# Kernel tuning notes

Hardware: AMD Instinct MI355X
Metric: run time of the kernel (lower is better)

Reference implementation:

```python
import jax, jax.numpy as jnp
import numpy as np

NUM_GROUPS = 4
DIVERSITY_STRENGTH = -0.5   # module stores -diversity_strength
DIVERSITY_DISCOUNT = 0.5
CAND_MULT = 1
N_GRAM = 2


def setup_inputs() -> dict:
    key = jax.random.key(0)
    k1, k2, k3, k5, k6 = jax.random.split(key, 5)
    bsz, beam, vocab, T = 64, 8, 50257, 128
    return {
        "lprobs": jax.random.normal(k1, (bsz, beam, vocab), jnp.float32),
        "scores": jax.random.normal(k2, (bsz, beam, T), jnp.float32),
        "group_overlap": jax.random.uniform(k3, (bsz, NUM_GROUPS, NUM_GROUPS), jnp.float32),
        "original_batch_idxs": jnp.arange(bsz, dtype=jnp.int32),
        "last_n_gram_indices": jax.random.randint(k5, (bsz, beam, N_GRAM - 1), 0, vocab, jnp.int32),
        "mask_last_n_gram_indices": jax.random.randint(k6, (bsz, beam, N_GRAM), 0, 2, jnp.int32),
        "step": 5,
    }


def reference(lprobs, scores, group_overlap, original_batch_idxs,
              last_n_gram_indices, mask_last_n_gram_indices, step):
    bsz, beam, vocab = lprobs.shape
    G = NUM_GROUPS
    mb = beam // G  # mini beam size
    k = CAND_MULT * mb
    batch_ar = jnp.arange(bsz)[:, None]

    scores_G, beams_G, idx_G = [], [], []
    for g in range(G):
        lp = lprobs[:, g::G, :]                       # [bsz, mb, vocab]
        sc = scores[:, g::G, step - 1]                # [bsz, mb]
        mk = mask_last_n_gram_indices[:, g::G, :]     # [bsz, mb, n_gram]
        if g > 0:
            # diversity penalty: scatter-add (1 + overlap) at previously picked tokens
            pen = 1.0 + group_overlap[original_batch_idxs, g, :g]          # [bsz, g]
            src = jnp.broadcast_to(pen[:, None, :], (bsz, mb, g)).reshape(bsz, -1)
            prev_idx = jnp.stack(idx_G, axis=-1).reshape(bsz, -1)          # [bsz, mb*g]
            div = jnp.zeros((bsz, vocab), lp.dtype).at[batch_ar, prev_idx].add(src)
            lp = lp + DIVERSITY_STRENGTH * div[:, None, :]
        # n-gram overlap mask: zero out beams whose mask rows are not all ones
        valid = (mk.sum(-1) == N_GRAM)                # [bsz, mb]
        lp = jnp.where(valid[:, :, None], lp, 0.0)
        # step > 0: add accumulated beam scores
        lp = lp + sc[:, :, None]
        flat = lp.reshape(bsz, -1)                    # [bsz, mb*vocab]
        top_idx = jax.lax.top_k(flat, k)[1]
        top_val = jnp.take_along_axis(flat, top_idx, axis=-1)
        beams_G.append((top_idx // vocab) * G + g)
        idx_G.append(top_idx % vocab)
        scores_G.append(top_val)

    scores_buf = jnp.stack(scores_G, axis=2).reshape(bsz, -1)   # [bsz, beam]
    indices_buf = jnp.stack(idx_G, axis=2).reshape(bsz, -1)
    beams_buf = jnp.stack(beams_G, axis=2).reshape(bsz, -1)

    # Hamming-cumulative overlap: [bsz, beam, n_gram] present n-grams, grouped
    present = jnp.concatenate(
        [last_n_gram_indices, indices_buf[:, :, None]], axis=-1
    ).reshape(bsz, mb, G, N_GRAM)
    eq = (present[:, :, None, :, :] == present[:, :, :, None, :])  # [bsz, mb, G, G, n]
    m = (mask_last_n_gram_indices != 0).reshape(bsz, mb, G, N_GRAM)
    om = m[:, :, None, :, :] & m[:, :, :, None, :]
    eq = jnp.where(om, eq, False)
    ov = (eq.sum(-1) == N_GRAM).astype(jnp.int32).sum(1)           # [bsz, G, G]

    new_group_overlap = (
        group_overlap.at[original_batch_idxs].add(ov.astype(group_overlap.dtype))
        * DIVERSITY_DISCOUNT
    )
    return scores_buf, indices_buf, beams_buf, new_group_overlap
```

## Files before the change

kernel.cpp:

```cpp
#include <hip/hip_runtime.h>
#include <math.h>

#define VOCAB 50257
#define BSZ   64
#define BEAM  8
#define NG    4
#define MB    2
#define KC    2
#define TLEN  128
#define NGRAM 2
#define SEG    64
#define SEGLEN 786
#define ROWS  (BSZ * BEAM)
#define CAP   1024

__device__ __forceinline__ bool better(float v1, int i1, float v2, int i2) {
    return (v1 > v2) || (v1 == v2 && i1 < i2);
}

struct Top2 { float v1, v2; int i1, i2; };

__device__ __forceinline__ void t2_init(Top2& t) {
    t.v1 = -INFINITY; t.v2 = -INFINITY; t.i1 = 0x7FFFFFFF; t.i2 = 0x7FFFFFFF;
}

__device__ __forceinline__ void t2_push(Top2& t, float v, int i) {
    if (better(v, i, t.v2, t.i2)) {
        if (better(v, i, t.v1, t.i1)) { t.v2 = t.v1; t.i2 = t.i1; t.v1 = v; t.i1 = i; }
        else                          { t.v2 = v;    t.i2 = i; }
    }
}

__device__ __forceinline__ void t2_merge(Top2& a, const Top2& b) {
    if (better(b.v1, b.i1, a.v1, a.i1)) {
        float nv2; int ni2;
        if (better(a.v1, a.i1, b.v2, b.i2)) { nv2 = a.v1; ni2 = a.i1; }
        else                                { nv2 = b.v2; ni2 = b.i2; }
        a.v1 = b.v1; a.i1 = b.i1; a.v2 = nv2; a.i2 = ni2;
    } else {
        if (better(b.v1, b.i1, a.v2, a.i2)) { a.v2 = b.v1; a.i2 = b.i1; }
    }
}

__device__ __forceinline__ float max4(float4 v) {
    return fmaxf(fmaxf(v.x, v.y), fmaxf(v.z, v.w));
}

__global__ __launch_bounds__(1024) void dbs_candidates(
    const float* __restrict__ lprobs,
    const int*   __restrict__ mask,
    int*   __restrict__ wscnt,
    float* __restrict__ wscv,
    int*   __restrict__ wsci)
{
    const int r    = blockIdx.x;
    const int tid  = threadIdx.x;
    const int w    = tid >> 6, lane = tid & 63;

    if (mask[r * NGRAM] + mask[r * NGRAM + 1] != NGRAM) return;

    __shared__ float s_max[SEG];
    __shared__ float s_tau;
    __shared__ int   s_cnt;
    __shared__ float s_cv[CAP];
    __shared__ int   s_ci[CAP];

    if (tid == 0) s_cnt = 0;

    const size_t rowoff = (size_t)r * VOCAB;
    const float* row = lprobs + rowoff;

    #pragma unroll
    for (int s = 0; s < 4; ++s) {
        const int seg   = w * 4 + s;
        const int start = seg * SEGLEN;
        const int end   = min(start + SEGLEN, VOCAB);
        const int mis   = (int)((rowoff + start) & 3);
        const int pre   = (4 - mis) & 3;

        float m = -INFINITY;
        if (lane < pre && start + lane < end) m = row[start + lane];
        const int vstart = start + pre;
        const int n4 = (end > vstart) ? ((end - vstart) >> 2) : 0;
        const float4* vrow = (const float4*)(row + vstart);

        float a0 = -INFINITY, a1 = -INFINITY, a2 = -INFINITY, a3 = -INFINITY;
        if (lane       < n4) a0 = max4(vrow[lane]);
        if (lane +  64 < n4) a1 = max4(vrow[lane + 64]);
        if (lane + 128 < n4) a2 = max4(vrow[lane + 128]);
        if (lane + 192 < n4) a3 = max4(vrow[lane + 192]);
        m = fmaxf(m, fmaxf(fmaxf(a0, a1), fmaxf(a2, a3)));
        const int tstart = vstart + 4 * n4;
        if (tstart + lane < end) m = fmaxf(m, row[tstart + lane]);

        #pragma unroll
        for (int off = 32; off > 0; off >>= 1) m = fmaxf(m, __shfl_xor(m, off));
        if (lane == 0) s_max[seg] = m;
    }
    __syncthreads();

    if (w == 0) {
        const float mym = s_max[lane];
        int rank = 0;
        for (int i = 0; i < SEG; ++i) {
            const float om = __shfl(mym, i);
            rank += better(om, i, mym, lane) ? 1 : 0;
        }
        if (rank == 7) s_tau = mym;
    }
    __syncthreads();
    const float tau = s_tau;

    #pragma unroll
    for (int s = 0; s < 4; ++s) {
        const int seg   = w * 4 + s;
        const int start = seg * SEGLEN;
        const int end   = min(start + SEGLEN, VOCAB);
        const int mis   = (int)((rowoff + start) & 3);
        const int pre   = (4 - mis) & 3;

        if (lane < pre && start + lane < end) {
            const float v = row[start + lane];
            if (v >= tau) {
                const int p = atomicAdd(&s_cnt, 1);
                if (p < CAP) { s_cv[p] = v; s_ci[p] = start + lane; }
            }
        }
        const int vstart = start + pre;
        const int n4 = (end > vstart) ? ((end - vstart) >> 2) : 0;
        const float4* vrow = (const float4*)(row + vstart);

        #pragma unroll
        for (int u = 0; u < 4; ++u) {
            const int jj = lane + u * 64;
            if (jj < n4) {
                const float4 v = vrow[jj];
                if (max4(v) >= tau) {
                    const int base = vstart + 4 * jj;
                    #pragma unroll
                    for (int e = 0; e < 4; ++e) {
                        const float ve = (e == 0) ? v.x : (e == 1) ? v.y
                                       : (e == 2) ? v.z : v.w;
                        if (ve >= tau) {
                            const int p = atomicAdd(&s_cnt, 1);
                            if (p < CAP) { s_cv[p] = ve; s_ci[p] = base + e; }
                        }
                    }
                }
            }
        }
        const int tstart = vstart + 4 * n4;
        if (tstart + lane < end) {
            const float v = row[tstart + lane];
            if (v >= tau) {
                const int p = atomicAdd(&s_cnt, 1);
                if (p < CAP) { s_cv[p] = v; s_ci[p] = tstart + lane; }
            }
        }
    }
    __syncthreads();

    const int cnt = min(s_cnt, CAP);
    if (tid == 0) wscnt[r] = cnt;
    for (int c = tid; c < cnt; c += 1024) {
        wscv[(size_t)r * CAP + c] = s_cv[c];
        wsci[(size_t)r * CAP + c] = s_ci[c];
    }
}

__global__ __launch_bounds__(64) void dbs_final(
    const float* __restrict__ scores,
    const float* __restrict__ overlap,
    const int*   __restrict__ obi,
    const int*   __restrict__ lastn,
    const int*   __restrict__ mask,
    const int*   __restrict__ stepp,
    const int*   __restrict__ wscnt,
    const float* __restrict__ wscv,
    const int*   __restrict__ wsci,
    float*       __restrict__ out)
{
    const int b   = blockIdx.x;
    const int tid = threadIdx.x;
    const int step = stepp[0];
    const int ob   = obi[b];

    __shared__ float s_sc[BEAM];
    __shared__ int   s_valid[BEAM];
    __shared__ float s_pen[(NG-1)*KC];
    __shared__ int   s_penidx[(NG-1)*KC];
    __shared__ float s_selv[NG][KC];
    __shared__ int   s_seli[NG][KC];
    __shared__ int   s_selm[NG][KC];

    if (tid < BEAM) {
        const int* mk = mask + ((size_t)b * BEAM + tid) * NGRAM;
        s_valid[tid] = (mk[0] + mk[1]) == NGRAM;
        s_sc[tid]    = scores[((size_t)b * BEAM + tid) * TLEN + (step - 1)];
    }
    __syncthreads();

    for (int g = 0; g < NG; ++g) {
        if (tid == 0) {
            for (int j = 0; j < g; ++j) {
                const float pen = 1.0f + overlap[((size_t)ob * NG + g) * NG + j];
                s_penidx[j*KC + 0] = s_seli[j][0]; s_pen[j*KC + 0] = pen;
                s_penidx[j*KC + 1] = s_seli[j][1]; s_pen[j*KC + 1] = pen;
            }
        }
        __syncthreads();

        const int np = KC * g;
        Top2 t; t2_init(t);
        for (int m = 0; m < MB; ++m) {
            const int beam = m * NG + g;
            if (s_valid[beam]) {
                const int r = b * BEAM + beam;
                const int n = wscnt[r];
                for (int c = tid; c < n; c += 64) {
                    const float v   = wscv[(size_t)r * CAP + c];
                    const int   idx = wsci[(size_t)r * CAP + c];
                    float dv = 0.0f;
                    #pragma unroll
                    for (int p = 0; p < (NG-1)*KC; ++p)
                        if (p < np && s_penidx[p] == idx) dv += s_pen[p];
                    t2_push(t, v - 0.5f * dv + s_sc[beam], m * VOCAB + idx);
                }
            } else if (tid < KC) {
                t2_push(t, s_sc[beam], m * VOCAB + tid);
            }
        }

        #pragma unroll
        for (int off = 32; off > 0; off >>= 1) {
            Top2 o;
            o.v1 = __shfl_down(t.v1, off); o.i1 = __shfl_down(t.i1, off);
            o.v2 = __shfl_down(t.v2, off); o.i2 = __shfl_down(t.i2, off);
            t2_merge(t, o);
        }
        if (tid == 0) {
            s_selv[g][0] = t.v1; s_seli[g][0] = t.i1 % VOCAB; s_selm[g][0] = t.i1 / VOCAB;
            s_selv[g][1] = t.v2; s_seli[g][1] = t.i2 % VOCAB; s_selm[g][1] = t.i2 / VOCAB;
        }
        __syncthreads();
    }

    if (tid < KC * NG) {
        const int i = tid;
        const int m = i / NG, g = i % NG;
        out[(size_t)b * BEAM + i]        = s_selv[g][m];
        out[512 + (size_t)b * BEAM + i]  = (float)s_seli[g][m];
        out[1024 + (size_t)b * BEAM + i] = (float)(s_selm[g][m] * NG + g);
    }
    if (tid >= 16 && tid < 16 + NG * NG) {
        const int q  = tid - 16;
        const int g1 = q / NG, g2 = q % NG;
        int ov = 0;
        for (int m = 0; m < MB; ++m) {
            const int i1 = m * NG + g1, i2 = m * NG + g2;
            const int p1a = lastn[(size_t)b * BEAM + i1];
            const int p2a = lastn[(size_t)b * BEAM + i2];
            const int p1b = s_seli[g1][m];
            const int p2b = s_seli[g2][m];
            const int* mk1 = mask + ((size_t)b * BEAM + i1) * NGRAM;
            const int* mk2 = mask + ((size_t)b * BEAM + i2) * NGRAM;
            const bool e0 = (p1a == p2a) && (mk1[0] != 0) && (mk2[0] != 0);
            const bool e1 = (p1b == p2b) && (mk1[1] != 0) && (mk2[1] != 0);
            ov += (e0 && e1) ? 1 : 0;
        }
        out[1536 + (size_t)ob * (NG * NG) + q] =
            (overlap[(size_t)ob * (NG * NG) + q] + (float)ov) * 0.5f;
    }
}

extern "C" void kernel_launch(void* const* d_in, const int* in_sizes, int n_in,
                              void* d_out, int out_size, void* d_ws, size_t ws_size,
                              hipStream_t stream) {
    const float* lprobs  = (const float*)d_in[0];
    const float* scores  = (const float*)d_in[1];
    const float* overlap = (const float*)d_in[2];
    const int*   obi     = (const int*)d_in[3];
    const int*   lastn   = (const int*)d_in[4];
    const int*   mask    = (const int*)d_in[5];
    const int*   stepp   = (const int*)d_in[6];
    float*       out     = (float*)d_out;

    int*   wscnt = (int*)d_ws;
    float* wscv  = (float*)((char*)d_ws + ROWS * 4);
    int*   wsci  = (int*)((char*)d_ws + ROWS * 4 + (size_t)ROWS * CAP * 4);

    dbs_candidates<<<ROWS, 1024, 0, stream>>>(lprobs, mask, wscnt, wscv, wsci);
    dbs_final     <<<BSZ, 64, 0, stream>>>(scores, overlap, obi, lastn, mask, stepp,
                                           wscnt, wscv, wsci, out);
}
```

Before: 27.20 us.

## Split each row's candidate filtering across four 256-thread blocks

Instead of one 1024-thread block per row computing a threshold over 64 segments, each row is now handled by four 256-thread blocks, each covering 16 segments with its own local threshold (8th-largest segment max) and its own candidate buffer. The final kernel then merges candidates from all four quarter-slots. The aim is finer-grained blocks for better CU occupancy and scheduling, and less shared memory per block. The cost is more candidates overall, since each quarter keeps at least 8 segments' worth, and a longer merge loop in the final kernel.

```diff
diff --git a/kernel.cpp b/kernel.cpp
--- a/kernel.cpp
+++ b/kernel.cpp
@@ -9,10 +9,11 @@
 #define KC    2
 #define TLEN  128
 #define NGRAM 2
-#define SEG    64
 #define SEGLEN 786
+#define QSEG  16
+#define NQ    4
 #define ROWS  (BSZ * BEAM)
-#define CAP   1024
+#define CAPQ  256
 
 __device__ __forceinline__ bool better(float v1, int i1, float v2, int i2) {
     return (v1 > v2) || (v1 == v2 && i1 < i2);
@@ -46,25 +47,27 @@
     return fmaxf(fmaxf(v.x, v.y), fmaxf(v.z, v.w));
 }
 
-__global__ __launch_bounds__(1024) void dbs_candidates(
+__global__ __launch_bounds__(256) void dbs_candidates(
     const float* __restrict__ lprobs,
     const int*   __restrict__ mask,
     int*   __restrict__ wscnt,
     float* __restrict__ wscv,
     int*   __restrict__ wsci)
 {
-    const int r    = blockIdx.x;
+    const int blk  = blockIdx.x;
+    const int r    = blk >> 2;
+    const int q    = blk & 3;
     const int tid  = threadIdx.x;
     const int w    = tid >> 6, lane = tid & 63;
 
-    if (mask[r * NGRAM] + mask[r * NGRAM + 1] != NGRAM) return;
-
-    __shared__ float s_max[SEG];
+    const int2 mk = *(const int2*)(mask + r * NGRAM);
+    if (mk.x + mk.y != NGRAM) return;
+
+    __shared__ float s_max[QSEG];
     __shared__ float s_tau;
     __shared__ int   s_cnt;
-    __shared__ float s_cv[CAP];
-    __shared__ int   s_ci[CAP];
-
+    __shared__ float s_cv[CAPQ];
+    __shared__ int   s_ci[CAPQ];
     if (tid == 0) s_cnt = 0;
 
     const size_t rowoff = (size_t)r * VOCAB;
@@ -72,8 +75,8 @@
 
     #pragma unroll
     for (int s = 0; s < 4; ++s) {
-        const int seg   = w * 4 + s;
-        const int start = seg * SEGLEN;
+        const int lseg  = w * 4 + s;
+        const int start = (q * QSEG + lseg) * SEGLEN;
         const int end   = min(start + SEGLEN, VOCAB);
         const int mis   = (int)((rowoff + start) & 3);
         const int pre   = (4 - mis) & 3;
@@ -95,26 +98,27 @@
 
         #pragma unroll
         for (int off = 32; off > 0; off >>= 1) m = fmaxf(m, __shfl_xor(m, off));
-        if (lane == 0) s_max[seg] = m;
+        if (lane == 0) s_max[lseg] = m;
     }
     __syncthreads();
 
     if (w == 0) {
-        const float mym = s_max[lane];
+        const float mym = (lane < QSEG) ? s_max[lane] : -INFINITY;
         int rank = 0;
-        for (int i = 0; i < SEG; ++i) {
+        #pragma unroll
+        for (int i = 0; i < QSEG; ++i) {
             const float om = __shfl(mym, i);
             rank += better(om, i, mym, lane) ? 1 : 0;
         }
-        if (rank == 7) s_tau = mym;
+        if (lane < QSEG && rank == 7) s_tau = mym;
     }
     __syncthreads();
     const float tau = s_tau;
 
     #pragma unroll
     for (int s = 0; s < 4; ++s) {
-        const int seg   = w * 4 + s;
-        const int start = seg * SEGLEN;
+        const int lseg  = w * 4 + s;
+        const int start = (q * QSEG + lseg) * SEGLEN;
         const int end   = min(start + SEGLEN, VOCAB);
         const int mis   = (int)((rowoff + start) & 3);
         const int pre   = (4 - mis) & 3;
@@ -123,7 +127,7 @@
             const float v = row[start + lane];
             if (v >= tau) {
                 const int p = atomicAdd(&s_cnt, 1);
-                if (p < CAP) { s_cv[p] = v; s_ci[p] = start + lane; }
+                if (p < CAPQ) { s_cv[p] = v; s_ci[p] = start + lane; }
             }
         }
         const int vstart = start + pre;
@@ -143,7 +147,7 @@
                                        : (e == 2) ? v.z : v.w;
                         if (ve >= tau) {
                             const int p = atomicAdd(&s_cnt, 1);
-                            if (p < CAP) { s_cv[p] = ve; s_ci[p] = base + e; }
+                            if (p < CAPQ) { s_cv[p] = ve; s_ci[p] = base + e; }
                         }
                     }
                 }
@@ -154,17 +158,18 @@
             const float v = row[tstart + lane];
             if (v >= tau) {
                 const int p = atomicAdd(&s_cnt, 1);
-                if (p < CAP) { s_cv[p] = v; s_ci[p] = tstart + lane; }
+                if (p < CAPQ) { s_cv[p] = v; s_ci[p] = tstart + lane; }
             }
         }
     }
     __syncthreads();
 
-    const int cnt = min(s_cnt, CAP);
-    if (tid == 0) wscnt[r] = cnt;
-    for (int c = tid; c < cnt; c += 1024) {
-        wscv[(size_t)r * CAP + c] = s_cv[c];
-        wsci[(size_t)r * CAP + c] = s_ci[c];
+    const int cnt  = min(s_cnt, CAPQ);
+    const int slot = r * NQ + q;
+    if (tid == 0) wscnt[slot] = cnt;
+    for (int c = tid; c < cnt; c += 256) {
+        wscv[(size_t)slot * CAPQ + c] = s_cv[c];
+        wsci[(size_t)slot * CAPQ + c] = s_ci[c];
     }
 }
 
@@ -216,15 +221,18 @@
             const int beam = m * NG + g;
             if (s_valid[beam]) {
                 const int r = b * BEAM + beam;
-                const int n = wscnt[r];
-                for (int c = tid; c < n; c += 64) {
-                    const float v   = wscv[(size_t)r * CAP + c];
-                    const int   idx = wsci[(size_t)r * CAP + c];
-                    float dv = 0.0f;
-                    #pragma unroll
-                    for (int p = 0; p < (NG-1)*KC; ++p)
-                        if (p < np && s_penidx[p] == idx) dv += s_pen[p];
-                    t2_push(t, v - 0.5f * dv + s_sc[beam], m * VOCAB + idx);
+                for (int qq = 0; qq < NQ; ++qq) {
+                    const int slot = r * NQ + qq;
+                    const int n = wscnt[slot];
+                    for (int c = tid; c < n; c += 64) {
+                        const float v   = wscv[(size_t)slot * CAPQ + c];
+                        const int   idx = wsci[(size_t)slot * CAPQ + c];
+                        float dv = 0.0f;
+                        #pragma unroll
+                        for (int p = 0; p < (NG-1)*KC; ++p)
+                            if (p < np && s_penidx[p] == idx) dv += s_pen[p];
+                        t2_push(t, v - 0.5f * dv + s_sc[beam], m * VOCAB + idx);
+                    }
                 }
             } else if (tid < KC) {
                 t2_push(t, s_sc[beam], m * VOCAB + tid);
@@ -286,10 +294,11 @@
     float*       out     = (float*)d_out;
 
     int*   wscnt = (int*)d_ws;
-    float* wscv  = (float*)((char*)d_ws + ROWS * 4);
-    int*   wsci  = (int*)((char*)d_ws + ROWS * 4 + (size_t)ROWS * CAP * 4);
-
-    dbs_candidates<<<ROWS, 1024, 0, stream>>>(lprobs, mask, wscnt, wscv, wsci);
+    float* wscv  = (float*)((char*)d_ws + (size_t)ROWS * NQ * 4);
+    int*   wsci  = (int*)((char*)d_ws + (size_t)ROWS * NQ * 4
+                          + (size_t)ROWS * NQ * CAPQ * 4);
+
+    dbs_candidates<<<ROWS * NQ, 256, 0, stream>>>(lprobs, mask, wscnt, wscv, wsci);
     dbs_final     <<<BSZ, 64, 0, stream>>>(scores, overlap, obi, lastn, mask, stepp,
                                            wscnt, wscv, wsci, out);
 }
```

After: 39.43 us. 45.0% more time.
